# Kernel tuning notes

Measured on AMD Instinct MI355X. Metric: run time of the kernel, lower is better.

## Reference

```python
import jax, jax.numpy as jnp
import numpy as np

E, H, I, K, T = 8, 1024, 2816, 2, 2048


def setup_inputs() -> dict:
    key = jax.random.key(0)
    k1, k2, k3, k4, k5, k6 = jax.random.split(key, 6)
    hidden_states = jax.random.normal(k1, (T, H), dtype=jnp.float32)
    top_k_indices = jax.random.randint(k2, (T, K), 0, E, dtype=jnp.int32)
    raw = jax.random.uniform(k3, (T, K), dtype=jnp.float32) + 0.1
    top_k_values = raw / jnp.sum(raw, axis=-1, keepdims=True)  # router softmax-like weights
    scale = 1.0 / np.sqrt(H)
    w_gate = jax.random.normal(k4, (E, H, I), dtype=jnp.float32) * scale
    w_up = jax.random.normal(k5, (E, H, I), dtype=jnp.float32) * scale
    w_down = jax.random.normal(k6, (E, I, H), dtype=jnp.float32) * (1.0 / np.sqrt(I))
    return {
        "hidden_states": hidden_states,
        "top_k_indices": top_k_indices,
        "top_k_values": top_k_values,
        "w_gate": w_gate,
        "w_up": w_up,
        "w_down": w_down,
    }


def reference(hidden_states, top_k_indices, top_k_values, w_gate, w_up, w_down):
    # Each expert: SwiGLU FFN  down( silu(x @ gate) * (x @ up) )
    # Run every expert on every token (dense reference for grouped-GEMM dispatch),
    # then combine with the per-token top-k routing weights.
    def expert(wg, wu, wd):
        g = jnp.matmul(hidden_states, wg)          # [T, I]
        u = jnp.matmul(hidden_states, wu)          # [T, I]
        return jnp.matmul(jax.nn.silu(g) * u, wd)  # [T, H]

    y = jax.vmap(expert)(w_gate, w_up, w_down)     # [E, T, H]

    t = hidden_states.shape[0]
    # comb[t, e] = sum over k of top_k_values[t, k] where top_k_indices[t, k] == e
    comb = jnp.zeros((t, w_gate.shape[0]), dtype=hidden_states.dtype)
    comb = comb.at[jnp.arange(t)[:, None], top_k_indices].add(top_k_values)
    out = jnp.einsum('te,eth->th', comb, y)        # weighted combine -> [T, H]
    return out
```

## Files before the change

### kernel.cpp

```cpp
#include <hip/hip_runtime.h>
#include <stdint.h>

#define T_TOK 2048
#define KTOP  2
#define NEXP  8
#define HDIM  1024
#define IDIM  2816

#define NPAIR 4096

#define BM        128
#define MAX_TILES 40
#define NPP       (NPAIR + BM)
#define BN2       128
#define BK2       32
#define BN3       64
#define BK3       64

#define R1BM   256
#define R1T    24
#define R1NPP  (NPAIR + R1BM)
#define R1BN2  128
#define R1BK2  32
#define R1BKp2 40
#define R1BN3  64
#define R1BK3  64
#define R1BKp3 72

typedef __attribute__((ext_vector_type(8))) short short8;
typedef __attribute__((ext_vector_type(4))) float floatx4;

__device__ __forceinline__ unsigned short f2bf(float f) {
  unsigned int u = __float_as_uint(f);
  u += 0x7fffu + ((u >> 16) & 1u);
  return (unsigned short)(u >> 16);
}

__device__ __forceinline__ void glds16(const unsigned short* g, unsigned short* l) {
  __builtin_amdgcn_global_load_lds(
      (const __attribute__((address_space(1))) unsigned int*)g,
      (__attribute__((address_space(3))) unsigned int*)l, 16, 0, 0);
}

__global__ void setup_kernel(const int* __restrict__ idx,
                             const float* __restrict__ vals,
                             int* __restrict__ hdr,
                             int* __restrict__ stok,
                             float* __restrict__ sw, int bm) {
  __shared__ int cnt[NEXP];
  __shared__ int off[NEXP];
  int tid = threadIdx.x;
  if (tid < NEXP) cnt[tid] = 0;
  __syncthreads();
  for (int p = tid; p < NPAIR; p += blockDim.x) atomicAdd(&cnt[idx[p]], 1);
  __syncthreads();
  if (tid == 0) {
    int s = 0, nt = 0;
    for (int e = 0; e < NEXP; ++e) {
      off[e] = s;
      int n = cnt[e];
      for (int t0 = 0; t0 < n; t0 += bm) {
        hdr[nt] = e;
        hdr[64 + nt] = s + t0;
        hdr[128 + nt] = s + n;
        nt++;
      }
      s += n;
    }
    for (; nt < 64; ++nt) hdr[nt] = -1;
  }
  __syncthreads();
  for (int p = tid; p < NPAIR; p += blockDim.x) {
    int e = idx[p];
    int pos = atomicAdd(&off[e], 1);
    stok[pos] = p / KTOP;
    sw[pos] = vals[p];
  }
}

__global__ void gather_kernel(const float* __restrict__ hidden,
                              const int* __restrict__ stok,
                              unsigned short* __restrict__ Xs) {
  int p = blockIdx.x;
  int t = stok[p];
  const float4* src = reinterpret_cast<const float4*>(hidden + (size_t)t * HDIM);
  float4 v = src[threadIdx.x];
  uint2 q;
  q.x = f2bf(v.x) | ((unsigned)f2bf(v.y) << 16);
  q.y = f2bf(v.z) | ((unsigned)f2bf(v.w) << 16);
  *reinterpret_cast<uint2*>(Xs + (size_t)p * HDIM + threadIdx.x * 4) = q;
}

__global__ __launch_bounds__(256) void convert_kernel(
    const float* __restrict__ wg, const float* __restrict__ wu,
    const float* __restrict__ wd, unsigned short* __restrict__ wgT,
    unsigned short* __restrict__ wuT, unsigned short* __restrict__ wdT,
    int zoff) {
  __shared__ float ls[64][65];
  int z = blockIdx.z + zoff;
  int e = blockIdx.y;
  int M = (z == 2) ? IDIM : HDIM;
  int N = (z == 2) ? HDIM : IDIM;
  const float* src = (z == 0 ? wg : z == 1 ? wu : wd) + (size_t)e * M * N;
  unsigned short* dst = (z == 0 ? wgT : z == 1 ? wuT : wdT) + (size_t)e * M * N;
  int ntx = N >> 6;
  int n0 = (blockIdx.x % ntx) << 6;
  int m0 = (blockIdx.x / ntx) << 6;
  int t = threadIdx.x;
  int rr = t >> 4, cc = (t & 15) * 4;
#pragma unroll
  for (int i = 0; i < 4; ++i) {
    int r = rr + i * 16;
    float4 v = *reinterpret_cast<const float4*>(src + (size_t)(m0 + r) * N + n0 + cc);
    ls[r][cc] = v.x; ls[r][cc + 1] = v.y; ls[r][cc + 2] = v.z; ls[r][cc + 3] = v.w;
  }
  __syncthreads();
  int mc = (t & 7) * 8, nn = t >> 3;
#pragma unroll
  for (int i = 0; i < 2; ++i) {
    int n = nn + i * 32;
    uint4 q;
    q.x = f2bf(ls[mc][n])     | ((unsigned)f2bf(ls[mc + 1][n]) << 16);
    q.y = f2bf(ls[mc + 2][n]) | ((unsigned)f2bf(ls[mc + 3][n]) << 16);
    q.z = f2bf(ls[mc + 4][n]) | ((unsigned)f2bf(ls[mc + 5][n]) << 16);
    q.w = f2bf(ls[mc + 6][n]) | ((unsigned)f2bf(ls[mc + 7][n]) << 16);
    *reinterpret_cast<uint4*>(dst + (size_t)(n0 + n) * M + m0 + mc) = q;
  }
}

__global__ __launch_bounds__(256, 2) void gateup_kernel(
    const unsigned short* __restrict__ Xs, const unsigned short* __restrict__ wgT,
    const unsigned short* __restrict__ wuT, const int* __restrict__ hdr,
    const float* __restrict__ sw_g, unsigned short* __restrict__ Act) {
  int bx = blockIdx.x;
  int e = hdr[bx];
  if (e < 0) return;
  int row0 = hdr[64 + bx];
  int rowlim = hdr[128 + bx] - row0;
  int n0 = blockIdx.y * BN2;

  __shared__ __align__(16) unsigned short As[BM * BK2];
  __shared__ __align__(16) unsigned short Bg[BN2 * BK2];
  __shared__ __align__(16) unsigned short Bu[BN2 * BK2];
  __shared__ float sw[BM];

  int tid = threadIdx.x, lane = tid & 63, wave = tid >> 6;
  if (tid < BM) sw[tid] = sw_g[row0 + tid];

  const unsigned short* wgb = wgT + (size_t)e * IDIM * HDIM;
  const unsigned short* wub = wuT + (size_t)e * IDIM * HDIM;

  floatx4 accg[4][4], accu[4][4];
  floatx4 zz = {0.f, 0.f, 0.f, 0.f};
#pragma unroll
  for (int a = 0; a < 4; ++a)
#pragma unroll
    for (int b = 0; b < 4; ++b) { accg[a][b] = zz; accu[a][b] = zz; }

  int wm = (wave >> 1) * 64, wn = (wave & 1) * 64;
  int lr = lane >> 2;
  int lk = (((lane & 3) ^ ((lr >> 1) & 3)) * 8);
  int fr = lane & 15;
  int fq = (((lane >> 4) ^ ((fr >> 1) & 3)) * 8);

  for (int kb = 0; kb < HDIM; kb += BK2) {
#pragma unroll
    for (int it = 0; it < 2; ++it) {
      int c = wave * 2 + it;
      glds16(Xs  + (size_t)(row0 + c * 16 + lr) * HDIM + kb + lk, &As[c * 512]);
      glds16(wgb + (size_t)(n0  + c * 16 + lr) * HDIM + kb + lk, &Bg[c * 512]);
      glds16(wub + (size_t)(n0  + c * 16 + lr) * HDIM + kb + lk, &Bu[c * 512]);
    }
    __syncthreads();

    short8 af[4], bg8[4], bu8[4];
#pragma unroll
    for (int x = 0; x < 4; ++x) {
      af[x]  = *reinterpret_cast<const short8*>(&As[(wm + x * 16 + fr) * BK2 + fq]);
      bg8[x] = *reinterpret_cast<const short8*>(&Bg[(wn + x * 16 + fr) * BK2 + fq]);
      bu8[x] = *reinterpret_cast<const short8*>(&Bu[(wn + x * 16 + fr) * BK2 + fq]);
    }
#pragma unroll
    for (int tm = 0; tm < 4; ++tm)
#pragma unroll
      for (int tn = 0; tn < 4; ++tn) {
        accg[tm][tn] = __builtin_amdgcn_mfma_f32_16x16x32_bf16(af[tm], bg8[tn], accg[tm][tn], 0, 0, 0);
        accu[tm][tn] = __builtin_amdgcn_mfma_f32_16x16x32_bf16(af[tm], bu8[tn], accu[tm][tn], 0, 0, 0);
      }
    __syncthreads();
  }

#pragma unroll
  for (int tm = 0; tm < 4; ++tm)
#pragma unroll
    for (int tn = 0; tn < 4; ++tn)
#pragma unroll
      for (int r = 0; r < 4; ++r) {
        int rl = wm + tm * 16 + (lane >> 4) * 4 + r;
        if (rl < rowlim) {
          int col = n0 + wn + tn * 16 + fr;
          float g = accg[tm][tn][r];
          float u = accu[tm][tn][r];
          float s = g / (1.f + __expf(-g));
          Act[(size_t)(row0 + rl) * IDIM + col] = f2bf(s * u * sw[rl]);
        }
      }
}

__global__ __launch_bounds__(256, 3) void down_kernel(
    const unsigned short* __restrict__ Act, const unsigned short* __restrict__ wdT,
    const int* __restrict__ hdr, const int* __restrict__ stok,
    float* __restrict__ out) {
  int bx = blockIdx.x;
  int e = hdr[bx];
  if (e < 0) return;
  int row0 = hdr[64 + bx];
  int rowlim = hdr[128 + bx] - row0;
  int n0 = blockIdx.y * BN3;

  __shared__ __align__(16) unsigned short As[BM * BK3];
  __shared__ __align__(16) unsigned short Bd[BN3 * BK3];
  __shared__ int stk[BM];

  int tid = threadIdx.x, lane = tid & 63, wave = tid >> 6;
  if (tid < BM) stk[tid] = stok[row0 + tid];

  const unsigned short* wdb = wdT + (size_t)e * HDIM * IDIM;

  floatx4 acc[4][2];
  floatx4 zz = {0.f, 0.f, 0.f, 0.f};
#pragma unroll
  for (int a = 0; a < 4; ++a) { acc[a][0] = zz; acc[a][1] = zz; }

  int wm = (wave >> 1) * 64, wn = (wave & 1) * 32;
  int lr8 = lane >> 3;
  int lk8 = (((lane & 7) ^ lr8) * 8);
  int fr = lane & 15;
  int fk = fr & 7;

  for (int kb = 0; kb < IDIM; kb += BK3) {
#pragma unroll
    for (int it = 0; it < 4; ++it) {
      int c = wave * 4 + it;
      glds16(Act + (size_t)(row0 + c * 8 + lr8) * IDIM + kb + lk8, &As[c * 512]);
    }
#pragma unroll
    for (int it = 0; it < 2; ++it) {
      int c = wave * 2 + it;
      glds16(wdb + (size_t)(n0 + c * 8 + lr8) * IDIM + kb + lk8, &Bd[c * 512]);
    }
    __syncthreads();

#pragma unroll
    for (int ks = 0; ks < BK3; ks += 32) {
      int q8 = (ks >> 3) + (lane >> 4);
      int fo = ((q8 ^ fk) * 8);
      short8 af[4], bd8[2];
#pragma unroll
      for (int x = 0; x < 4; ++x)
        af[x] = *reinterpret_cast<const short8*>(&As[(wm + x * 16 + fr) * BK3 + fo]);
#pragma unroll
      for (int x = 0; x < 2; ++x)
        bd8[x] = *reinterpret_cast<const short8*>(&Bd[(wn + x * 16 + fr) * BK3 + fo]);
#pragma unroll
      for (int tm = 0; tm < 4; ++tm)
#pragma unroll
        for (int tn = 0; tn < 2; ++tn)
          acc[tm][tn] = __builtin_amdgcn_mfma_f32_16x16x32_bf16(af[tm], bd8[tn], acc[tm][tn], 0, 0, 0);
    }
    __syncthreads();
  }

#pragma unroll
  for (int tm = 0; tm < 4; ++tm)
#pragma unroll
    for (int tn = 0; tn < 2; ++tn)
#pragma unroll
      for (int r = 0; r < 4; ++r) {
        int rl = wm + tm * 16 + (lane >> 4) * 4 + r;
        if (rl < rowlim) {
          int col = n0 + wn + tn * 16 + fr;
          unsafeAtomicAdd(&out[(size_t)stk[rl] * HDIM + col], acc[tm][tn][r]);
        }
      }
}

__global__ __launch_bounds__(512, 2) void gateup_fb(
    const unsigned short* __restrict__ Xs, const float* __restrict__ wg,
    const float* __restrict__ wu, const int* __restrict__ hdr,
    const float* __restrict__ sw_g, unsigned short* __restrict__ Act) {
  int by = blockIdx.y;
  int e = hdr[by];
  if (e < 0) return;
  int row0 = hdr[64 + by];
  int row_end = hdr[128 + by];
  int n0 = blockIdx.x * R1BN2;

  __shared__ __align__(16) unsigned short As[R1BM * R1BKp2];
  __shared__ __align__(16) unsigned short Bg[R1BN2 * R1BKp2];
  __shared__ __align__(16) unsigned short Bu[R1BN2 * R1BKp2];
  __shared__ float sw[R1BM];

  int tid = threadIdx.x, lane = tid & 63, wave = tid >> 6;
  if (tid < R1BM) sw[tid] = sw_g[row0 + tid];

  const float* wgb = wg + (size_t)e * HDIM * IDIM;
  const float* wub = wu + (size_t)e * HDIM * IDIM;

  floatx4 accg[4][4], accu[4][4];
  floatx4 zz = {0.f, 0.f, 0.f, 0.f};
#pragma unroll
  for (int a = 0; a < 4; ++a)
#pragma unroll
    for (int b = 0; b < 4; ++b) { accg[a][b] = zz; accu[a][b] = zz; }

  int wm = (wave >> 1) * 64, wn = (wave & 1) * 64;

  for (int kb = 0; kb < HDIM; kb += R1BK2) {
    __syncthreads();
#pragma unroll
    for (int it = 0; it < 2; ++it) {
      int cc = wave * 2 + it;
      int m = cc * 16 + (lane >> 2);
      int k = (lane & 3) * 8;
      uint4 v = *reinterpret_cast<const uint4*>(Xs + (size_t)(row0 + m) * HDIM + kb + k);
      *reinterpret_cast<uint4*>(&As[m * R1BKp2 + k]) = v;
    }
#pragma unroll
    for (int it = 0; it < 2; ++it) {
      int cc = wave * 2 + it;
      const float* wb = (cc & 8) ? wub : wgb;
      unsigned short* Bs = (cc & 8) ? Bu : Bg;
      int r = cc & 7;
      int kblk = r >> 1, nh = r & 1;
      int n = nh * 64 + lane;
      int k = kblk * 8;
      const float* src = wb + (size_t)(kb + k) * IDIM + n0 + n;
      uint4 q;
      q.x = f2bf(src[0])                | ((unsigned)f2bf(src[(size_t)IDIM])     << 16);
      q.y = f2bf(src[2 * (size_t)IDIM]) | ((unsigned)f2bf(src[3 * (size_t)IDIM]) << 16);
      q.z = f2bf(src[4 * (size_t)IDIM]) | ((unsigned)f2bf(src[5 * (size_t)IDIM]) << 16);
      q.w = f2bf(src[6 * (size_t)IDIM]) | ((unsigned)f2bf(src[7 * (size_t)IDIM]) << 16);
      *reinterpret_cast<uint4*>(&Bs[n * R1BKp2 + k]) = q;
    }
    __syncthreads();

    int krd = (lane >> 4) * 8;
    short8 af[4], bgf[4], buf_[4];
#pragma unroll
    for (int tm = 0; tm < 4; ++tm)
      af[tm] = *reinterpret_cast<const short8*>(&As[(wm + tm * 16 + (lane & 15)) * R1BKp2 + krd]);
#pragma unroll
    for (int tn = 0; tn < 4; ++tn) {
      bgf[tn]  = *reinterpret_cast<const short8*>(&Bg[(wn + tn * 16 + (lane & 15)) * R1BKp2 + krd]);
      buf_[tn] = *reinterpret_cast<const short8*>(&Bu[(wn + tn * 16 + (lane & 15)) * R1BKp2 + krd]);
    }
#pragma unroll
    for (int tm = 0; tm < 4; ++tm)
#pragma unroll
      for (int tn = 0; tn < 4; ++tn) {
        accg[tm][tn] = __builtin_amdgcn_mfma_f32_16x16x32_bf16(af[tm], bgf[tn], accg[tm][tn], 0, 0, 0);
        accu[tm][tn] = __builtin_amdgcn_mfma_f32_16x16x32_bf16(af[tm], buf_[tn], accu[tm][tn], 0, 0, 0);
      }
  }

  int rowlim = row_end - row0;
#pragma unroll
  for (int tm = 0; tm < 4; ++tm)
#pragma unroll
    for (int tn = 0; tn < 4; ++tn)
#pragma unroll
      for (int r = 0; r < 4; ++r) {
        int rl = wm + tm * 16 + (lane >> 4) * 4 + r;
        if (rl < rowlim) {
          int col = n0 + wn + tn * 16 + (lane & 15);
          float g = accg[tm][tn][r];
          float u = accu[tm][tn][r];
          float s = g / (1.f + __expf(-g));
          Act[(size_t)(row0 + rl) * IDIM + col] = f2bf(s * u * sw[rl]);
        }
      }
}

__global__ __launch_bounds__(512, 2) void down_fb(
    const unsigned short* __restrict__ Act, const float* __restrict__ wd,
    const int* __restrict__ hdr, const int* __restrict__ stok,
    float* __restrict__ out) {
  int by = blockIdx.y;
  int e = hdr[by];
  if (e < 0) return;
  int row0 = hdr[64 + by];
  int row_end = hdr[128 + by];
  int n0 = blockIdx.x * R1BN3;

  __shared__ __align__(16) unsigned short As[R1BM * R1BKp3];
  __shared__ __align__(16) unsigned short Bd[R1BN3 * R1BKp3];
  __shared__ int stk[R1BM];

  int tid = threadIdx.x, lane = tid & 63, wave = tid >> 6;
  if (tid < R1BM) stk[tid] = stok[row0 + tid];

  const float* wdb = wd + (size_t)e * IDIM * HDIM;

  floatx4 acc[4][2];
  floatx4 zz = {0.f, 0.f, 0.f, 0.f};
#pragma unroll
  for (int a = 0; a < 4; ++a) { acc[a][0] = zz; acc[a][1] = zz; }

  int wm = (wave >> 1) * 64, wn = (wave & 1) * 32;

  for (int kb = 0; kb < IDIM; kb += R1BK3) {
    __syncthreads();
#pragma unroll
    for (int it = 0; it < 4; ++it) {
      int cc = wave * 4 + it;
      int m = cc * 8 + (lane >> 3);
      int k = (lane & 7) * 8;
      uint4 v = *reinterpret_cast<const uint4*>(Act + (size_t)(row0 + m) * IDIM + kb + k);
      *reinterpret_cast<uint4*>(&As[m * R1BKp3 + k]) = v;
    }
    {
      int n = lane;
      int k = wave * 8;
      const float* src = wdb + (size_t)(kb + k) * HDIM + n0 + n;
      uint4 q;
      q.x = f2bf(src[0])        | ((unsigned)f2bf(src[HDIM])     << 16);
      q.y = f2bf(src[2 * HDIM]) | ((unsigned)f2bf(src[3 * HDIM]) << 16);
      q.z = f2bf(src[4 * HDIM]) | ((unsigned)f2bf(src[5 * HDIM]) << 16);
      q.w = f2bf(src[6 * HDIM]) | ((unsigned)f2bf(src[7 * HDIM]) << 16);
      *reinterpret_cast<uint4*>(&Bd[n * R1BKp3 + k]) = q;
    }
    __syncthreads();

#pragma unroll
    for (int ks = 0; ks < R1BK3; ks += 32) {
      int krd = ks + (lane >> 4) * 8;
      short8 af[4], bdf[2];
#pragma unroll
      for (int tm = 0; tm < 4; ++tm)
        af[tm] = *reinterpret_cast<const short8*>(&As[(wm + tm * 16 + (lane & 15)) * R1BKp3 + krd]);
#pragma unroll
      for (int tn = 0; tn < 2; ++tn)
        bdf[tn] = *reinterpret_cast<const short8*>(&Bd[(wn + tn * 16 + (lane & 15)) * R1BKp3 + krd]);
#pragma unroll
      for (int tm = 0; tm < 4; ++tm)
#pragma unroll
        for (int tn = 0; tn < 2; ++tn)
          acc[tm][tn] = __builtin_amdgcn_mfma_f32_16x16x32_bf16(af[tm], bdf[tn], acc[tm][tn], 0, 0, 0);
    }
  }

  int rowlim = row_end - row0;
#pragma unroll
  for (int tm = 0; tm < 4; ++tm)
#pragma unroll
    for (int tn = 0; tn < 2; ++tn)
#pragma unroll
      for (int r = 0; r < 4; ++r) {
        int rl = wm + tm * 16 + (lane >> 4) * 4 + r;
        if (rl < rowlim) {
          int col = n0 + wn + tn * 16 + (lane & 15);
          unsafeAtomicAdd(&out[(size_t)stk[rl] * HDIM + col], acc[tm][tn][r]);
        }
      }
}

extern "C" void kernel_launch(void* const* d_in, const int* in_sizes, int n_in,
                              void* d_out, int out_size, void* d_ws, size_t ws_size,
                              hipStream_t stream) {
  const float* hidden = (const float*)d_in[0];
  const int* idx = (const int*)d_in[1];
  const float* vals = (const float*)d_in[2];
  const float* wg = (const float*)d_in[3];
  const float* wu = (const float*)d_in[4];
  const float* wd = (const float*)d_in[5];
  float* out = (float*)d_out;
  char* ws = (char*)d_ws;

  hipMemsetAsync(d_out, 0, (size_t)out_size * sizeof(float), stream);

  const size_t OFF_STOK = 4096;
  const size_t OFF_SW   = OFF_STOK + (size_t)NPP * 4;
  const size_t OFF_XS   = 65536;
  const size_t OFF_ACT  = OFF_XS + (size_t)NPP * HDIM * 2;
  const size_t OFF_WG   = OFF_ACT + (size_t)NPP * IDIM * 2;
  const size_t WSZ      = (size_t)NEXP * HDIM * IDIM * 2;
  const size_t OFF_WU   = OFF_WG + WSZ;
  const size_t NEED     = OFF_WU + WSZ;

  if (ws_size >= NEED) {
    int* hdr = (int*)ws;
    int* stok = (int*)(ws + OFF_STOK);
    float* sw = (float*)(ws + OFF_SW);
    unsigned short* Xs  = (unsigned short*)(ws + OFF_XS);
    unsigned short* Act = (unsigned short*)(ws + OFF_ACT);
    unsigned short* wgT = (unsigned short*)(ws + OFF_WG);
    unsigned short* wuT = (unsigned short*)(ws + OFF_WU);
    unsigned short* wdT = wgT;

    setup_kernel<<<1, 256, 0, stream>>>(idx, vals, hdr, stok, sw, BM);
    convert_kernel<<<dim3(704, NEXP, 2), 256, 0, stream>>>(wg, wu, wd, wgT, wuT, wdT, 0);
    gather_kernel<<<NPAIR, 256, 0, stream>>>(hidden, stok, Xs);
    gateup_kernel<<<dim3(MAX_TILES, IDIM / BN2), 256, 0, stream>>>(Xs, wgT, wuT, hdr, sw, Act);
    convert_kernel<<<dim3(704, NEXP, 1), 256, 0, stream>>>(wg, wu, wd, wgT, wuT, wdT, 2);
    down_kernel<<<dim3(MAX_TILES, HDIM / BN3), 256, 0, stream>>>(Act, wdT, hdr, stok, out);
  } else {
    int* hdr = (int*)ws;
    int* stok = (int*)(ws + 4096);
    float* sw = (float*)(ws + 4096 + (size_t)R1NPP * 4);
    unsigned short* Xs  = (unsigned short*)(ws + 65536);
    unsigned short* Act = (unsigned short*)(ws + 65536 + (size_t)R1NPP * HDIM * 2);

    setup_kernel<<<1, 256, 0, stream>>>(idx, vals, hdr, stok, sw, R1BM);
    gather_kernel<<<NPAIR, 256, 0, stream>>>(hidden, stok, Xs);
    gateup_fb<<<dim3(IDIM / R1BN2, R1T), 512, 0, stream>>>(Xs, wg, wu, hdr, sw, Act);
    down_fb<<<dim3(HDIM / R1BN3, R1T), 512, 0, stream>>>(Act, wd, hdr, stok, out);
  }
}
```

Measured before the change: 452.9 us.

## Double-buffer LDS tiles in gate/up and down GEMMs, merge weight conversions

```diff
diff --git a/kernel.cpp b/kernel.cpp
--- a/kernel.cpp
+++ b/kernel.cpp
@@ -128,7 +128,7 @@
   }
 }
 
-__global__ __launch_bounds__(256, 2) void gateup_kernel(
+__global__ __launch_bounds__(256, 3) void gateup_kernel(
     const unsigned short* __restrict__ Xs, const unsigned short* __restrict__ wgT,
     const unsigned short* __restrict__ wuT, const int* __restrict__ hdr,
     const float* __restrict__ sw_g, unsigned short* __restrict__ Act) {
@@ -139,9 +139,9 @@
   int rowlim = hdr[128 + bx] - row0;
   int n0 = blockIdx.y * BN2;
 
-  __shared__ __align__(16) unsigned short As[BM * BK2];
-  __shared__ __align__(16) unsigned short Bg[BN2 * BK2];
-  __shared__ __align__(16) unsigned short Bu[BN2 * BK2];
+  __shared__ __align__(16) unsigned short As[2][BM * BK2];
+  __shared__ __align__(16) unsigned short Bg[2][BN2 * BK2];
+  __shared__ __align__(16) unsigned short Bu[2][BN2 * BK2];
   __shared__ float sw[BM];
 
   int tid = threadIdx.x, lane = tid & 63, wave = tid >> 6;
@@ -163,22 +163,28 @@
   int fr = lane & 15;
   int fq = (((lane >> 4) ^ ((fr >> 1) & 3)) * 8);
 
-  for (int kb = 0; kb < HDIM; kb += BK2) {
+  auto stage = [&](int p, int kb) {
 #pragma unroll
     for (int it = 0; it < 2; ++it) {
       int c = wave * 2 + it;
-      glds16(Xs  + (size_t)(row0 + c * 16 + lr) * HDIM + kb + lk, &As[c * 512]);
-      glds16(wgb + (size_t)(n0  + c * 16 + lr) * HDIM + kb + lk, &Bg[c * 512]);
-      glds16(wub + (size_t)(n0  + c * 16 + lr) * HDIM + kb + lk, &Bu[c * 512]);
-    }
+      glds16(Xs  + (size_t)(row0 + c * 16 + lr) * HDIM + kb + lk, &As[p][c * 512]);
+      glds16(wgb + (size_t)(n0  + c * 16 + lr) * HDIM + kb + lk, &Bg[p][c * 512]);
+      glds16(wub + (size_t)(n0  + c * 16 + lr) * HDIM + kb + lk, &Bu[p][c * 512]);
+    }
+  };
+
+  stage(0, 0);
+  int p = 0;
+  for (int kb = 0; kb < HDIM; kb += BK2) {
     __syncthreads();
+    if (kb + BK2 < HDIM) stage(p ^ 1, kb + BK2);
 
     short8 af[4], bg8[4], bu8[4];
 #pragma unroll
     for (int x = 0; x < 4; ++x) {
-      af[x]  = *reinterpret_cast<const short8*>(&As[(wm + x * 16 + fr) * BK2 + fq]);
-      bg8[x] = *reinterpret_cast<const short8*>(&Bg[(wn + x * 16 + fr) * BK2 + fq]);
-      bu8[x] = *reinterpret_cast<const short8*>(&Bu[(wn + x * 16 + fr) * BK2 + fq]);
+      af[x]  = *reinterpret_cast<const short8*>(&As[p][(wm + x * 16 + fr) * BK2 + fq]);
+      bg8[x] = *reinterpret_cast<const short8*>(&Bg[p][(wn + x * 16 + fr) * BK2 + fq]);
+      bu8[x] = *reinterpret_cast<const short8*>(&Bu[p][(wn + x * 16 + fr) * BK2 + fq]);
     }
 #pragma unroll
     for (int tm = 0; tm < 4; ++tm)
@@ -187,7 +193,7 @@
         accg[tm][tn] = __builtin_amdgcn_mfma_f32_16x16x32_bf16(af[tm], bg8[tn], accg[tm][tn], 0, 0, 0);
         accu[tm][tn] = __builtin_amdgcn_mfma_f32_16x16x32_bf16(af[tm], bu8[tn], accu[tm][tn], 0, 0, 0);
       }
-    __syncthreads();
+    p ^= 1;
   }
 
 #pragma unroll
@@ -218,8 +224,8 @@
   int rowlim = hdr[128 + bx] - row0;
   int n0 = blockIdx.y * BN3;
 
-  __shared__ __align__(16) unsigned short As[BM * BK3];
-  __shared__ __align__(16) unsigned short Bd[BN3 * BK3];
+  __shared__ __align__(16) unsigned short As[2][BM * BK3];
+  __shared__ __align__(16) unsigned short Bd[2][BN3 * BK3];
   __shared__ int stk[BM];
 
   int tid = threadIdx.x, lane = tid & 63, wave = tid >> 6;
@@ -238,18 +244,24 @@
   int fr = lane & 15;
   int fk = fr & 7;
 
-  for (int kb = 0; kb < IDIM; kb += BK3) {
+  auto stage = [&](int p, int kb) {
 #pragma unroll
     for (int it = 0; it < 4; ++it) {
       int c = wave * 4 + it;
-      glds16(Act + (size_t)(row0 + c * 8 + lr8) * IDIM + kb + lk8, &As[c * 512]);
+      glds16(Act + (size_t)(row0 + c * 8 + lr8) * IDIM + kb + lk8, &As[p][c * 512]);
     }
 #pragma unroll
     for (int it = 0; it < 2; ++it) {
       int c = wave * 2 + it;
-      glds16(wdb + (size_t)(n0 + c * 8 + lr8) * IDIM + kb + lk8, &Bd[c * 512]);
-    }
+      glds16(wdb + (size_t)(n0 + c * 8 + lr8) * IDIM + kb + lk8, &Bd[p][c * 512]);
+    }
+  };
+
+  stage(0, 0);
+  int p = 0;
+  for (int kb = 0; kb < IDIM; kb += BK3) {
     __syncthreads();
+    if (kb + BK3 < IDIM) stage(p ^ 1, kb + BK3);
 
 #pragma unroll
     for (int ks = 0; ks < BK3; ks += 32) {
@@ -258,17 +270,17 @@
       short8 af[4], bd8[2];
 #pragma unroll
       for (int x = 0; x < 4; ++x)
-        af[x] = *reinterpret_cast<const short8*>(&As[(wm + x * 16 + fr) * BK3 + fo]);
+        af[x] = *reinterpret_cast<const short8*>(&As[p][(wm + x * 16 + fr) * BK3 + fo]);
 #pragma unroll
       for (int x = 0; x < 2; ++x)
-        bd8[x] = *reinterpret_cast<const short8*>(&Bd[(wn + x * 16 + fr) * BK3 + fo]);
+        bd8[x] = *reinterpret_cast<const short8*>(&Bd[p][(wn + x * 16 + fr) * BK3 + fo]);
 #pragma unroll
       for (int tm = 0; tm < 4; ++tm)
 #pragma unroll
         for (int tn = 0; tn < 2; ++tn)
           acc[tm][tn] = __builtin_amdgcn_mfma_f32_16x16x32_bf16(af[tm], bd8[tn], acc[tm][tn], 0, 0, 0);
     }
-    __syncthreads();
+    p ^= 1;
   }
 
 #pragma unroll
@@ -486,7 +498,9 @@
   const size_t OFF_WG   = OFF_ACT + (size_t)NPP * IDIM * 2;
   const size_t WSZ      = (size_t)NEXP * HDIM * IDIM * 2;
   const size_t OFF_WU   = OFF_WG + WSZ;
-  const size_t NEED     = OFF_WU + WSZ;
+  const size_t OFF_WD   = OFF_WU + WSZ;
+  const size_t NEED     = OFF_WD;
+  const size_t NEED2    = OFF_WD + WSZ;
 
   if (ws_size >= NEED) {
     int* hdr = (int*)ws;
@@ -496,14 +510,22 @@
     unsigned short* Act = (unsigned short*)(ws + OFF_ACT);
     unsigned short* wgT = (unsigned short*)(ws + OFF_WG);
     unsigned short* wuT = (unsigned short*)(ws + OFF_WU);
-    unsigned short* wdT = wgT;
 
     setup_kernel<<<1, 256, 0, stream>>>(idx, vals, hdr, stok, sw, BM);
-    convert_kernel<<<dim3(704, NEXP, 2), 256, 0, stream>>>(wg, wu, wd, wgT, wuT, wdT, 0);
     gather_kernel<<<NPAIR, 256, 0, stream>>>(hidden, stok, Xs);
-    gateup_kernel<<<dim3(MAX_TILES, IDIM / BN2), 256, 0, stream>>>(Xs, wgT, wuT, hdr, sw, Act);
-    convert_kernel<<<dim3(704, NEXP, 1), 256, 0, stream>>>(wg, wu, wd, wgT, wuT, wdT, 2);
-    down_kernel<<<dim3(MAX_TILES, HDIM / BN3), 256, 0, stream>>>(Act, wdT, hdr, stok, out);
+
+    if (ws_size >= NEED2) {
+      unsigned short* wdT = (unsigned short*)(ws + OFF_WD);
+      convert_kernel<<<dim3(704, NEXP, 3), 256, 0, stream>>>(wg, wu, wd, wgT, wuT, wdT, 0);
+      gateup_kernel<<<dim3(MAX_TILES, IDIM / BN2), 256, 0, stream>>>(Xs, wgT, wuT, hdr, sw, Act);
+      down_kernel<<<dim3(MAX_TILES, HDIM / BN3), 256, 0, stream>>>(Act, wdT, hdr, stok, out);
+    } else {
+      unsigned short* wdT = wgT;
+      convert_kernel<<<dim3(704, NEXP, 2), 256, 0, stream>>>(wg, wu, wd, wgT, wuT, wdT, 0);
+      gateup_kernel<<<dim3(MAX_TILES, IDIM / BN2), 256, 0, stream>>>(Xs, wgT, wuT, hdr, sw, Act);
+      convert_kernel<<<dim3(704, NEXP, 1), 256, 0, stream>>>(wg, wu, wd, wgT, wuT, wdT, 2);
+      down_kernel<<<dim3(MAX_TILES, HDIM / BN3), 256, 0, stream>>>(Act, wdT, hdr, stok, out);
+    }
   } else {
     int* hdr = (int*)ws;
     int* stok = (int*)(ws + 4096);
```

Result: slower. 643.9 us (+42.2%).
